# Performance work log

Measured on AMD Instinct MI355X. Metric: run time of the kernel, lower is better.

## Reference

```python
import jax, jax.numpy as jnp
import numpy as np

TH, TL = 0.85, 0.5          # sim thresholds
ALPHA = 0.1                 # proto EMA alpha
TEMP = 1.0                  # readout temperature
KEEP, REFINE, REPLACE, SPAWN = 0, 1, 2, 3


def _l2n(x, axis=-1):
    return x / jnp.maximum(jnp.linalg.norm(x, axis=axis, keepdims=True), 1e-12)


def setup_inputs() -> dict:
    key = jax.random.key(0)
    ks = jax.random.split(key, 12)
    B, N, C, H, W, K = 4, 8, 256, 64, 64, 16
    return {
        "value_BNCHW": jax.random.normal(ks[0], (B, N, C, H, W), jnp.float32),
        "frame_feat_BCHW": jax.random.normal(ks[1], (B, C, H, W), jnp.float32),
        "mask_BNHW": jax.random.uniform(ks[2], (B, N, H, W), jnp.float32),
        "proto": jax.random.normal(ks[3], (B, N, K, C), jnp.float32),
        "age": jax.random.uniform(ks[4], (B, N, K), jnp.float32) * 10.0,
        "usage": jax.random.uniform(ks[5], (B, N, K), jnp.float32) * 5.0,
        "conf": jax.random.uniform(ks[6], (B, N, K), jnp.float32),
        "valid": jax.random.bernoulli(ks[7], 0.7, (B, N, K)),
        "W1": jax.random.normal(ks[8], (C + K + 3 * K, 256), jnp.float32) * 0.02,
        "b1": jnp.zeros((256,), jnp.float32),
        "W2": jax.random.normal(ks[9], (256, 4), jnp.float32) * 0.02,
        "b2": jnp.zeros((4,), jnp.float32),
        "proto_gate": jnp.float32(1.0),
        "frame_gate": jnp.float32(1.0),
    }


def reference(value_BNCHW, frame_feat_BCHW, mask_BNHW, proto, age, usage, conf,
              valid, W1, b1, W2, b2, proto_gate, frame_gate):
    B, N, C, H, W = value_BNCHW.shape
    K = proto.shape[2]
    P = H * W

    # ---- candidate prototype: masked mean pool over HW ----
    flat_v = value_BNCHW.reshape(B, N, C, P)          # [B,N,C,P]
    flat_m = mask_BNHW.reshape(B, N, 1, P)            # [B,N,1,P]
    denom = flat_m.sum(-1)                            # [B,N,1]
    cand = (flat_v * flat_m).sum(-1) / jnp.maximum(denom, 1e-6)
    fallback = flat_v.mean(-1)
    cand = jnp.where(denom <= 1e-5, fallback, cand)   # [B,N,C]
    mask_strength = flat_m.mean(-1)[..., 0]           # [B,N]
    cand = _l2n(cand)

    # ---- cosine sim against bank + context ----
    norm_bank = _l2n(proto)
    sim = jnp.einsum('bnc,bnkc->bnk', cand, norm_bank)
    sim = jnp.where(valid, sim, -1.0)
    g_t = frame_feat_BCHW.mean((2, 3))                # [B,C]
    age_n = age / jnp.maximum(jax.lax.stop_gradient(age.max()), 1.0)
    use_n = usage / jnp.maximum(jax.lax.stop_gradient(usage.max()), 1.0)
    stats = jnp.stack([age_n, use_n, conf], -1).reshape(B, N, 3 * K)
    context = jnp.concatenate(
        [jnp.broadcast_to(g_t[:, None, :], (B, N, C)), sim, stats], -1)
    any_valid = valid.any(-1)
    target_slot = jnp.where(any_valid, sim.argmax(-1), 0)
    max_sim = jnp.take_along_axis(sim, target_slot[..., None], -1)[..., 0]
    max_sim = jnp.where(any_valid, max_sim, 0.0)

    # ---- policy MLP (logits logged; rule-based policy selects action) ----
    logits = jax.nn.gelu(context @ W1 + b1) @ W2 + b2  # [B,N,4]

    has_free = (~valid).any(-1)
    low = max_sim < TL
    action = jnp.full((B, N), REFINE, jnp.int32)
    action = jnp.where(max_sim > TH, KEEP, action)
    action = jnp.where(low & has_free, SPAWN, action)
    action = jnp.where(low & ~has_free, REPLACE, action)

    # ---- action-conditioned slot selection + scatter update ----
    worst = jnp.argmax(age - usage - conf + 1000.0 * (~valid), -1)
    free_slot = jnp.argmax(~valid, -1)
    spawn = action == SPAWN
    replace = action == REPLACE
    refine = action == REFINE
    keep = action == KEEP
    chosen = target_slot
    chosen = jnp.where(spawn & has_free, free_slot, chosen)
    chosen = jnp.where(spawn & ~has_free, worst, chosen)   # spawn_replace_when_full
    chosen = jnp.where(replace, worst, chosen)
    update = refine | replace | spawn
    replace_like = replace | spawn

    bi = jnp.arange(B)[:, None]
    ni = jnp.arange(N)[None, :]

    old_p = proto[bi, ni, chosen]                      # [B,N,C] gather
    refined = _l2n((1.0 - ALPHA) * old_p + ALPHA * cand)
    new_p = jnp.where(refine[..., None], refined,
                      jnp.where(replace_like[..., None], cand, old_p))
    proto_new = proto.at[bi, ni, chosen].set(new_p)

    age1 = age + 1.0
    age_new = age1.at[bi, ni, chosen].set(
        jnp.where(replace_like, 0.0, age1[bi, ni, chosen]))
    usage_new = usage.at[bi, ni, chosen].set(
        jnp.where(replace_like, 1.0,
                  usage[bi, ni, chosen] + (refine | keep).astype(jnp.float32)))
    conf_g = conf[bi, ni, chosen]
    conf_val = jnp.where(refine, jnp.clip(0.5 * conf_g + 0.5 * max_sim, 0.0, 1.0),
                         jnp.where(replace_like, jnp.clip(mask_strength, 0.0, 1.0),
                                   conf_g))
    conf_new = conf.at[bi, ni, chosen].set(conf_val)
    valid_new = valid.at[bi, ni, chosen].set(valid[bi, ni, chosen] | update)

    # ---- prototype-conditioned readout (softmax over bank slots per pixel) ----
    vn = flat_v / jnp.maximum(jnp.linalg.norm(flat_v, axis=2, keepdims=True), 1e-12)
    nb = _l2n(proto_new)
    scores = jnp.einsum('bnkc,bncp->bnkp', nb, vn) / TEMP
    scores = jnp.where(valid_new[..., None], scores, -1e9)
    wts = jax.nn.softmax(scores, axis=2)               # over K
    proto_map = jnp.einsum('bnkp,bnkc->bncp', wts, proto_new)
    proto_map = jnp.where(valid_new.any(-1)[:, :, None, None], proto_map, 0.0)
    proto_map = proto_map.reshape(B, N, C, H, W)

    conditioned = (value_BNCHW + proto_gate * proto_map
                   + frame_gate * frame_feat_BCHW[:, None])
    return conditioned, logits
```

## Files before the change

kernel.cpp:

```cpp
#include <hip/hip_runtime.h>
#include <math.h>

#define NB_B 4
#define NB_N 8
#define NB_C 256
#define NB_K 16
#define NB_P 4096
#define NB_BN (NB_B * NB_N)

#define WS_WSUM 0
#define WS_VSUM (NB_BN * NB_C)
#define WS_GT   (2 * NB_BN * NB_C)
#define WS_DEN  (WS_GT + NB_B * NB_C)
#define WS_NB   17440
#define WS_PN   (WS_NB + NB_BN * NB_K * NB_C)
#define WS_VAL  (WS_PN + NB_BN * NB_K * NB_C)

__device__ __forceinline__ float2 blk_sum2(float a, float b, float2* sbuf) {
#pragma unroll
  for (int off = 32; off > 0; off >>= 1) {
    a += __shfl_down(a, off, 64);
    b += __shfl_down(b, off, 64);
  }
  int lane = threadIdx.x & 63, wid = threadIdx.x >> 6;
  __syncthreads();
  if (lane == 0) sbuf[wid] = make_float2(a, b);
  __syncthreads();
  float2 r;
  r.x = sbuf[0].x + sbuf[1].x + sbuf[2].x + sbuf[3].x;
  r.y = sbuf[0].y + sbuf[1].y + sbuf[2].y + sbuf[3].y;
  return r;
}

__device__ __forceinline__ float2 blk_max2(float a, float b, float2* sbuf) {
#pragma unroll
  for (int off = 32; off > 0; off >>= 1) {
    a = fmaxf(a, __shfl_down(a, off, 64));
    b = fmaxf(b, __shfl_down(b, off, 64));
  }
  int lane = threadIdx.x & 63, wid = threadIdx.x >> 6;
  __syncthreads();
  if (lane == 0) sbuf[wid] = make_float2(a, b);
  __syncthreads();
  float2 r;
  r.x = fmaxf(fmaxf(sbuf[0].x, sbuf[1].x), fmaxf(sbuf[2].x, sbuf[3].x));
  r.y = fmaxf(fmaxf(sbuf[0].y, sbuf[1].y), fmaxf(sbuf[2].y, sbuf[3].y));
  return r;
}

__device__ __forceinline__ int validMode(const void* vptr) {
  const unsigned int* w = (const unsigned int*)vptr;
  int mode = 0;
  for (int i = 0; i < 128; ++i) {
    unsigned int x = w[i];
    if (x == 0x3f800000u) return 2;
    if (x > 1u) mode = 1;
  }
  return mode;
}
__device__ __forceinline__ bool getValid(const void* vptr, int mode, int idx) {
  if (mode == 1) return ((const unsigned char*)vptr)[idx] != 0;
  if (mode == 2) return ((const float*)vptr)[idx] != 0.0f;
  return ((const int*)vptr)[idx] != 0;
}

__global__ __launch_bounds__(256) void k1_reduce(
    const float* __restrict__ value, const float* __restrict__ frame,
    const float* __restrict__ mask, float* __restrict__ ws) {
  __shared__ float2 sbuf[4];
  int gid = blockIdx.x, tid = threadIdx.x;
  if (gid < NB_BN * NB_C) {
    int bn = gid >> 8;
    const float4* v4 = (const float4*)(value + (size_t)gid * NB_P);
    const float4* m4 = (const float4*)(mask + (size_t)bn * NB_P);
    float wsum = 0.f, vsum = 0.f;
#pragma unroll
    for (int i = 0; i < NB_P / 4 / 256; ++i) {
      float4 a = v4[i * 256 + tid];
      float4 m = m4[i * 256 + tid];
      wsum += a.x * m.x + a.y * m.y + a.z * m.z + a.w * m.w;
      vsum += a.x + a.y + a.z + a.w;
    }
    float2 r = blk_sum2(wsum, vsum, sbuf);
    if (tid == 0) { ws[WS_WSUM + gid] = r.x; ws[WS_VSUM + gid] = r.y; }
  } else if (gid < NB_BN * NB_C + NB_B * NB_C) {
    int idx = gid - NB_BN * NB_C;
    const float4* f4 = (const float4*)(frame + (size_t)idx * NB_P);
    float s = 0.f;
#pragma unroll
    for (int i = 0; i < 4; ++i) {
      float4 a = f4[i * 256 + tid];
      s += a.x + a.y + a.z + a.w;
    }
    float2 r = blk_sum2(s, 0.f, sbuf);
    if (tid == 0) ws[WS_GT + idx] = r.x * (1.0f / NB_P);
  } else {
    int bn = gid - NB_BN * NB_C - NB_B * NB_C;
    const float4* m4 = (const float4*)(mask + (size_t)bn * NB_P);
    float s = 0.f;
#pragma unroll
    for (int i = 0; i < 4; ++i) {
      float4 a = m4[i * 256 + tid];
      s += a.x + a.y + a.z + a.w;
    }
    float2 r = blk_sum2(s, 0.f, sbuf);
    if (tid == 0) ws[WS_DEN + bn] = r.x;
  }
}

__global__ __launch_bounds__(256) void k2_policy(
    const float* __restrict__ proto, const float* __restrict__ age,
    const float* __restrict__ usage, const float* __restrict__ conf,
    const void* __restrict__ valid, const float* __restrict__ W1,
    const float* __restrict__ b1, const float* __restrict__ W2,
    const float* __restrict__ b2, float* __restrict__ ws,
    float* __restrict__ out_logits) {
  __shared__ float2 sbuf[4];
  __shared__ float s_cand[NB_C];
  __shared__ float s_sim[NB_K];
  __shared__ float s_invn[NB_K];
  __shared__ float s_ctx[NB_C + NB_K + 3 * NB_K];
  __shared__ int s_dec[4];

  int bn = blockIdx.x;
  int b = bn >> 3;
  int c = threadIdx.x;
  int vmode = validMode(valid);

  float denom = ws[WS_DEN + bn];
  float cand;
  if (denom <= 1e-5f) cand = ws[WS_VSUM + bn * NB_C + c] * (1.0f / NB_P);
  else                cand = ws[WS_WSUM + bn * NB_C + c] / fmaxf(denom, 1e-6f);
  float2 r0 = blk_sum2(cand * cand, 0.f, sbuf);
  cand *= 1.0f / fmaxf(sqrtf(r0.x), 1e-12f);
  s_cand[c] = cand;

  const float* pr = proto + (size_t)bn * NB_K * NB_C;
  for (int k = 0; k < NB_K; ++k) {
    float p = pr[k * NB_C + c];
    float2 rr = blk_sum2(p * p, p * cand, sbuf);
    if (c == 0) {
      float invk = 1.0f / fmaxf(sqrtf(rr.x), 1e-12f);
      s_invn[k] = invk;
      s_sim[k] = getValid(valid, vmode, bn * NB_K + k) ? rr.y * invk : -1.0f;
    }
  }

  float am = fmaxf(age[c], age[c + 256]);
  float um = fmaxf(usage[c], usage[c + 256]);
  float2 mx = blk_max2(am, um, sbuf);
  float age_max = fmaxf(mx.x, 1.0f);
  float use_max = fmaxf(mx.y, 1.0f);

  s_ctx[c] = ws[WS_GT + b * NB_C + c];
  if (c < NB_K) {
    int k = c;
    s_ctx[NB_C + k] = s_sim[k];
    s_ctx[NB_C + NB_K + 3 * k + 0] = age[bn * NB_K + k] / age_max;
    s_ctx[NB_C + NB_K + 3 * k + 1] = usage[bn * NB_K + k] / use_max;
    s_ctx[NB_C + NB_K + 3 * k + 2] = conf[bn * NB_K + k];
  }
  __syncthreads();

  float acc = b1[c];
  for (int i = 0; i < NB_C + 4 * NB_K; ++i) acc += s_ctx[i] * W1[i * 256 + c];
  float h = 0.5f * acc *
            (1.0f + tanhf(0.7978845608028654f * (acc + 0.044715f * acc * acc * acc)));
  for (int j = 0; j < 4; ++j) {
    float2 lj = blk_sum2(h * W2[c * 4 + j], 0.f, sbuf);
    if (c == 0) out_logits[bn * 4 + j] = lj.x + b2[j];
  }

  if (c == 0) {
    bool anyv = false, hasfree = false;
    for (int k = 0; k < NB_K; ++k) {
      if (getValid(valid, vmode, bn * NB_K + k)) anyv = true; else hasfree = true;
    }
    int tgt = 0; float best = s_sim[0];
    for (int k = 1; k < NB_K; ++k) if (s_sim[k] > best) { best = s_sim[k]; tgt = k; }
    if (!anyv) tgt = 0;
    float max_sim = anyv ? s_sim[tgt] : 0.0f;
    int action = 1;
    if (max_sim > 0.85f) action = 0;
    bool low = max_sim < 0.5f;
    if (low && hasfree) action = 3;
    if (low && !hasfree) action = 2;
    int worst = 0; float wb = -1e30f;
    for (int k = 0; k < NB_K; ++k) {
      float sc = age[bn * NB_K + k] - usage[bn * NB_K + k] - conf[bn * NB_K + k] +
                 (getValid(valid, vmode, bn * NB_K + k) ? 0.f : 1000.f);
      if (sc > wb) { wb = sc; worst = k; }
    }
    int freeslot = 0;
    for (int k = 0; k < NB_K; ++k) {
      if (!getValid(valid, vmode, bn * NB_K + k)) { freeslot = k; break; }
    }
    int chosen = tgt;
    if (action == 3) chosen = hasfree ? freeslot : worst;
    if (action == 2) chosen = worst;
    s_dec[0] = chosen;
    s_dec[1] = (action == 1);
    s_dec[2] = (action == 2 || action == 3);
    s_dec[3] = (action != 0);
  }
  __syncthreads();

  int chosen = s_dec[0];
  float oldp = pr[chosen * NB_C + c];
  float t = 0.9f * oldp + 0.1f * s_cand[c];
  float2 tn = blk_sum2(t * t, 0.f, sbuf);
  float invt = 1.0f / fmaxf(sqrtf(tn.x), 1e-12f);
  float pn_chosen = s_dec[1] ? t * invt
                   : (s_dec[2] ? s_cand[c]
                               : oldp);
  float nb_chosen = s_dec[1] ? t * invt
                   : (s_dec[2] ? s_cand[c]
                               : oldp * s_invn[chosen]);
  float* nbp = ws + WS_NB + (size_t)bn * NB_K * NB_C;
  float* pnp = ws + WS_PN + (size_t)bn * NB_K * NB_C;
  for (int k = 0; k < NB_K; ++k) {
    float praw = pr[k * NB_C + c];
    nbp[k * NB_C + c] = (k == chosen) ? nb_chosen : praw * s_invn[k];
    pnp[k * NB_C + c] = (k == chosen) ? pn_chosen : praw;
  }
  if (c < NB_K) {
    bool v = getValid(valid, vmode, bn * NB_K + c) || (c == chosen && s_dec[3]);
    ws[WS_VAL + bn * NB_K + c] = v ? 1.0f : 0.0f;
  }
}

__global__ __launch_bounds__(256) void k3_readout(
    const float* __restrict__ value, const float* __restrict__ frame,
    const float* __restrict__ ws, const float* __restrict__ pgp,
    const float* __restrict__ fgp, float* __restrict__ out) {
  __shared__ float s_nb[NB_C][NB_K];
  __shared__ float s_pn[NB_C][NB_K];
  int blk = blockIdx.x;
  int bn = blk >> 4, tile = blk & 15;
  int b = bn >> 3;
  int tid = threadIdx.x;
  int p = tile * 256 + tid;

  const float* nbp = ws + WS_NB + (size_t)bn * NB_K * NB_C;
  const float* pnp = ws + WS_PN + (size_t)bn * NB_K * NB_C;
  for (int i = tid; i < NB_K * NB_C; i += 256) {
    int k = i >> 8, c = i & 255;
    s_nb[c][k] = nbp[i];
    s_pn[c][k] = pnp[i];
  }
  int vmask = 0;
  for (int k = 0; k < NB_K; ++k)
    if (ws[WS_VAL + bn * NB_K + k] != 0.0f) vmask |= (1 << k);
  float pg = pgp[0], fg = fgp[0];
  __syncthreads();

  const float* vp = value + (size_t)bn * NB_C * NB_P + p;
  float d[NB_K];
#pragma unroll
  for (int k = 0; k < NB_K; ++k) d[k] = 0.f;
  float sumsq = 0.f;
#pragma unroll 4
  for (int c = 0; c < NB_C; ++c) {
    float v = vp[(size_t)c * NB_P];
    sumsq += v * v;
    const float4* nb4 = (const float4*)(&s_nb[c][0]);
    float4 n0 = nb4[0], n1 = nb4[1], n2 = nb4[2], n3 = nb4[3];
    d[0] += v * n0.x;  d[1] += v * n0.y;  d[2] += v * n0.z;  d[3] += v * n0.w;
    d[4] += v * n1.x;  d[5] += v * n1.y;  d[6] += v * n1.z;  d[7] += v * n1.w;
    d[8] += v * n2.x;  d[9] += v * n2.y;  d[10] += v * n2.z; d[11] += v * n2.w;
    d[12] += v * n3.x; d[13] += v * n3.y; d[14] += v * n3.z; d[15] += v * n3.w;
  }
  float invv = 1.0f / fmaxf(sqrtf(sumsq), 1e-12f);
  float m = -1e30f;
#pragma unroll
  for (int k = 0; k < NB_K; ++k) {
    d[k] *= invv;
    if ((vmask >> k) & 1) m = fmaxf(m, d[k]);
  }
  float w[NB_K]; float ssum = 0.f;
#pragma unroll
  for (int k = 0; k < NB_K; ++k) {
    float e = ((vmask >> k) & 1) ? __expf(d[k] - m) : 0.f;
    w[k] = e; ssum += e;
  }
  float isum = vmask ? (1.0f / ssum) : 0.0f;
#pragma unroll
  for (int k = 0; k < NB_K; ++k) w[k] *= isum;

  const float* fp = frame + (size_t)b * NB_C * NB_P + p;
  float* op = out + (size_t)bn * NB_C * NB_P + p;
#pragma unroll 2
  for (int c = 0; c < NB_C; ++c) {
    float v = vp[(size_t)c * NB_P];
    float f = fp[(size_t)c * NB_P];
    const float4* pn4 = (const float4*)(&s_pn[c][0]);
    float4 n0 = pn4[0], n1 = pn4[1], n2 = pn4[2], n3 = pn4[3];
    float pm = w[0] * n0.x + w[1] * n0.y + w[2] * n0.z + w[3] * n0.w +
               w[4] * n1.x + w[5] * n1.y + w[6] * n1.z + w[7] * n1.w +
               w[8] * n2.x + w[9] * n2.y + w[10] * n2.z + w[11] * n2.w +
               w[12] * n3.x + w[13] * n3.y + w[14] * n3.z + w[15] * n3.w;
    op[(size_t)c * NB_P] = v + pg * pm + fg * f;
  }
}

extern "C" void kernel_launch(void* const* d_in, const int* in_sizes, int n_in,
                              void* d_out, int out_size, void* d_ws, size_t ws_size,
                              hipStream_t stream) {
  const float* value = (const float*)d_in[0];
  const float* frame = (const float*)d_in[1];
  const float* mask  = (const float*)d_in[2];
  const float* proto = (const float*)d_in[3];
  const float* age   = (const float*)d_in[4];
  const float* usage = (const float*)d_in[5];
  const float* conf  = (const float*)d_in[6];
  const void*  valid = (const void*)d_in[7];
  const float* W1 = (const float*)d_in[8];
  const float* b1 = (const float*)d_in[9];
  const float* W2 = (const float*)d_in[10];
  const float* b2 = (const float*)d_in[11];
  const float* pg = (const float*)d_in[12];
  const float* fg = (const float*)d_in[13];
  float* out = (float*)d_out;
  float* ws = (float*)d_ws;

  int g1 = NB_BN * NB_C + NB_B * NB_C + NB_BN;
  hipLaunchKernelGGL(k1_reduce, dim3(g1), dim3(256), 0, stream,
                     value, frame, mask, ws);
  hipLaunchKernelGGL(k2_policy, dim3(NB_BN), dim3(256), 0, stream,
                     proto, age, usage, conf, valid, W1, b1, W2, b2, ws,
                     out + (size_t)NB_BN * NB_C * NB_P);
  hipLaunchKernelGGL(k3_readout, dim3(NB_BN * 16), dim3(256), 0, stream,
                     value, frame, ws, pg, fg, out);
}
```

Baseline: 150.2 us.

## Split readout channels across half-blocks and batch reduce rows per block

k1 now reduces four channel rows per block and reuses the mask loads across them, which cuts the block count and the number of mask reads. k3 now splits the 256 channels between two 128-thread halves, combines their partial dot products through shared memory, and doubles the grid to 1024 blocks for more parallelism. Shared memory is reused for the normalised and raw bank, the bank is stored channel-major so it loads with coalesced float4 copies, and the output is written with nontemporal stores. The cost is an extra shared-memory reduction step and added barriers in the readout.

Measured after the change: 161.3 us. 1.07x slower.

```diff
diff --git a/kernel.cpp b/kernel.cpp
--- a/kernel.cpp
+++ b/kernel.cpp
@@ -16,6 +16,24 @@
 #define WS_PN   (WS_NB + NB_BN * NB_K * NB_C)
 #define WS_VAL  (WS_PN + NB_BN * NB_K * NB_C)
 
+__device__ __forceinline__ void blk_sum8(float* a, float (*sbuf)[8]) {
+#pragma unroll
+  for (int off = 32; off > 0; off >>= 1) {
+#pragma unroll
+    for (int j = 0; j < 8; ++j) a[j] += __shfl_down(a[j], off, 64);
+  }
+  int lane = threadIdx.x & 63, wid = threadIdx.x >> 6;
+  __syncthreads();
+  if (lane == 0) {
+#pragma unroll
+    for (int j = 0; j < 8; ++j) sbuf[wid][j] = a[j];
+  }
+  __syncthreads();
+#pragma unroll
+  for (int j = 0; j < 8; ++j)
+    a[j] = sbuf[0][j] + sbuf[1][j] + sbuf[2][j] + sbuf[3][j];
+}
+
 __device__ __forceinline__ float2 blk_sum2(float a, float b, float2* sbuf) {
 #pragma unroll
   for (int off = 32; off > 0; off >>= 1) {
@@ -67,44 +85,70 @@
 __global__ __launch_bounds__(256) void k1_reduce(
     const float* __restrict__ value, const float* __restrict__ frame,
     const float* __restrict__ mask, float* __restrict__ ws) {
-  __shared__ float2 sbuf[4];
+  __shared__ float sbuf[4][8];
   int gid = blockIdx.x, tid = threadIdx.x;
-  if (gid < NB_BN * NB_C) {
-    int bn = gid >> 8;
-    const float4* v4 = (const float4*)(value + (size_t)gid * NB_P);
+  if (gid < 2048) {
+    int bn = gid >> 6, c0 = (gid & 63) << 2;
     const float4* m4 = (const float4*)(mask + (size_t)bn * NB_P);
-    float wsum = 0.f, vsum = 0.f;
-#pragma unroll
-    for (int i = 0; i < NB_P / 4 / 256; ++i) {
-      float4 a = v4[i * 256 + tid];
-      float4 m = m4[i * 256 + tid];
-      wsum += a.x * m.x + a.y * m.y + a.z * m.z + a.w * m.w;
-      vsum += a.x + a.y + a.z + a.w;
-    }
-    float2 r = blk_sum2(wsum, vsum, sbuf);
-    if (tid == 0) { ws[WS_WSUM + gid] = r.x; ws[WS_VSUM + gid] = r.y; }
-  } else if (gid < NB_BN * NB_C + NB_B * NB_C) {
-    int idx = gid - NB_BN * NB_C;
-    const float4* f4 = (const float4*)(frame + (size_t)idx * NB_P);
-    float s = 0.f;
-#pragma unroll
-    for (int i = 0; i < 4; ++i) {
-      float4 a = f4[i * 256 + tid];
-      s += a.x + a.y + a.z + a.w;
-    }
-    float2 r = blk_sum2(s, 0.f, sbuf);
-    if (tid == 0) ws[WS_GT + idx] = r.x * (1.0f / NB_P);
+    float4 mv[4];
+#pragma unroll
+    for (int i = 0; i < 4; ++i) mv[i] = m4[i * 256 + tid];
+    float acc[8];
+#pragma unroll
+    for (int r = 0; r < 4; ++r) {
+      const float4* v4 =
+          (const float4*)(value + ((size_t)bn * NB_C + c0 + r) * NB_P);
+      float wsum = 0.f, vsum = 0.f;
+#pragma unroll
+      for (int i = 0; i < 4; ++i) {
+        float4 a = v4[i * 256 + tid];
+        wsum += a.x * mv[i].x + a.y * mv[i].y + a.z * mv[i].z + a.w * mv[i].w;
+        vsum += a.x + a.y + a.z + a.w;
+      }
+      acc[2 * r] = wsum;
+      acc[2 * r + 1] = vsum;
+    }
+    blk_sum8(acc, sbuf);
+    if (tid == 0) {
+#pragma unroll
+      for (int r = 0; r < 4; ++r) {
+        ws[WS_WSUM + bn * NB_C + c0 + r] = acc[2 * r];
+        ws[WS_VSUM + bn * NB_C + c0 + r] = acc[2 * r + 1];
+      }
+    }
+  } else if (gid < 2048 + 256) {
+    int idx0 = (gid - 2048) << 2;
+    float acc[8] = {0.f, 0.f, 0.f, 0.f, 0.f, 0.f, 0.f, 0.f};
+#pragma unroll
+    for (int r = 0; r < 4; ++r) {
+      const float4* f4 = (const float4*)(frame + (size_t)(idx0 + r) * NB_P);
+      float s = 0.f;
+#pragma unroll
+      for (int i = 0; i < 4; ++i) {
+        float4 a = f4[i * 256 + tid];
+        s += a.x + a.y + a.z + a.w;
+      }
+      acc[r] = s;
+    }
+    blk_sum8(acc, sbuf);
+    if (tid == 0) {
+#pragma unroll
+      for (int r = 0; r < 4; ++r)
+        ws[WS_GT + idx0 + r] = acc[r] * (1.0f / NB_P);
+    }
   } else {
-    int bn = gid - NB_BN * NB_C - NB_B * NB_C;
+    int bn = gid - 2304;
     const float4* m4 = (const float4*)(mask + (size_t)bn * NB_P);
+    float acc[8] = {0.f, 0.f, 0.f, 0.f, 0.f, 0.f, 0.f, 0.f};
     float s = 0.f;
 #pragma unroll
     for (int i = 0; i < 4; ++i) {
       float4 a = m4[i * 256 + tid];
       s += a.x + a.y + a.z + a.w;
     }
-    float2 r = blk_sum2(s, 0.f, sbuf);
-    if (tid == 0) ws[WS_DEN + bn] = r.x;
+    acc[0] = s;
+    blk_sum8(acc, sbuf);
+    if (tid == 0) ws[WS_DEN + bn] = acc[0];
   }
 }
 
@@ -211,17 +255,15 @@
   float2 tn = blk_sum2(t * t, 0.f, sbuf);
   float invt = 1.0f / fmaxf(sqrtf(tn.x), 1e-12f);
   float pn_chosen = s_dec[1] ? t * invt
-                   : (s_dec[2] ? s_cand[c]
-                               : oldp);
+                   : (s_dec[2] ? s_cand[c] : oldp);
   float nb_chosen = s_dec[1] ? t * invt
-                   : (s_dec[2] ? s_cand[c]
-                               : oldp * s_invn[chosen]);
+                   : (s_dec[2] ? s_cand[c] : oldp * s_invn[chosen]);
   float* nbp = ws + WS_NB + (size_t)bn * NB_K * NB_C;
   float* pnp = ws + WS_PN + (size_t)bn * NB_K * NB_C;
   for (int k = 0; k < NB_K; ++k) {
     float praw = pr[k * NB_C + c];
-    nbp[k * NB_C + c] = (k == chosen) ? nb_chosen : praw * s_invn[k];
-    pnp[k * NB_C + c] = (k == chosen) ? pn_chosen : praw;
+    nbp[c * NB_K + k] = (k == chosen) ? nb_chosen : praw * s_invn[k];
+    pnp[c * NB_K + k] = (k == chosen) ? pn_chosen : praw;
   }
   if (c < NB_K) {
     bool v = getValid(valid, vmode, bn * NB_K + c) || (c == chosen && s_dec[3]);
@@ -229,47 +271,65 @@
   }
 }
 
-__global__ __launch_bounds__(256) void k3_readout(
+__global__ __launch_bounds__(256, 4) void k3_readout(
     const float* __restrict__ value, const float* __restrict__ frame,
     const float* __restrict__ ws, const float* __restrict__ pgp,
     const float* __restrict__ fgp, float* __restrict__ out) {
-  __shared__ float s_nb[NB_C][NB_K];
-  __shared__ float s_pn[NB_C][NB_K];
+  __shared__ float s_bank[NB_C * NB_K];
+  __shared__ float s_red[256 * 17];
   int blk = blockIdx.x;
-  int bn = blk >> 4, tile = blk & 15;
+  int bn = blk >> 5, tile = blk & 31;
   int b = bn >> 3;
   int tid = threadIdx.x;
-  int p = tile * 256 + tid;
-
-  const float* nbp = ws + WS_NB + (size_t)bn * NB_K * NB_C;
-  const float* pnp = ws + WS_PN + (size_t)bn * NB_K * NB_C;
-  for (int i = tid; i < NB_K * NB_C; i += 256) {
-    int k = i >> 8, c = i & 255;
-    s_nb[c][k] = nbp[i];
-    s_pn[c][k] = pnp[i];
-  }
+  int px = tid & 127, ch = tid >> 7;
+  int p0 = tile * 128;
+
+  const float4* nbp4 = (const float4*)(ws + WS_NB + (size_t)bn * NB_K * NB_C);
+  float4* sb4 = (float4*)s_bank;
+#pragma unroll
+  for (int j = 0; j < 4; ++j) sb4[j * 256 + tid] = nbp4[j * 256 + tid];
   int vmask = 0;
   for (int k = 0; k < NB_K; ++k)
     if (ws[WS_VAL + bn * NB_K + k] != 0.0f) vmask |= (1 << k);
   float pg = pgp[0], fg = fgp[0];
   __syncthreads();
 
-  const float* vp = value + (size_t)bn * NB_C * NB_P + p;
+  const float* vp = value + ((size_t)bn * NB_C + ch * 128) * NB_P + p0 + px;
+  const float* sbch = s_bank + ch * 128 * NB_K;
   float d[NB_K];
 #pragma unroll
   for (int k = 0; k < NB_K; ++k) d[k] = 0.f;
   float sumsq = 0.f;
-#pragma unroll 4
-  for (int c = 0; c < NB_C; ++c) {
+#pragma unroll 8
+  for (int c = 0; c < 128; ++c) {
     float v = vp[(size_t)c * NB_P];
     sumsq += v * v;
-    const float4* nb4 = (const float4*)(&s_nb[c][0]);
-    float4 n0 = nb4[0], n1 = nb4[1], n2 = nb4[2], n3 = nb4[3];
+    const float4* n4 = (const float4*)(sbch + c * NB_K);
+    float4 n0 = n4[0], n1 = n4[1], n2 = n4[2], n3 = n4[3];
     d[0] += v * n0.x;  d[1] += v * n0.y;  d[2] += v * n0.z;  d[3] += v * n0.w;
     d[4] += v * n1.x;  d[5] += v * n1.y;  d[6] += v * n1.z;  d[7] += v * n1.w;
     d[8] += v * n2.x;  d[9] += v * n2.y;  d[10] += v * n2.z; d[11] += v * n2.w;
     d[12] += v * n3.x; d[13] += v * n3.y; d[14] += v * n3.z; d[15] += v * n3.w;
   }
+  {
+    float* rr = s_red + tid * 17;
+#pragma unroll
+    for (int k = 0; k < NB_K; ++k) rr[k] = d[k];
+    rr[16] = sumsq;
+  }
+  __syncthreads();
+
+  const float4* pnp4 = (const float4*)(ws + WS_PN + (size_t)bn * NB_K * NB_C);
+#pragma unroll
+  for (int j = 0; j < 4; ++j) sb4[j * 256 + tid] = pnp4[j * 256 + tid];
+
+  {
+    const float* r0 = s_red + px * 17;
+    const float* r1 = s_red + (128 + px) * 17;
+#pragma unroll
+    for (int k = 0; k < NB_K; ++k) d[k] = r0[k] + r1[k];
+    sumsq = r0[16] + r1[16];
+  }
   float invv = 1.0f / fmaxf(sqrtf(sumsq), 1e-12f);
   float m = -1e30f;
 #pragma unroll
@@ -286,20 +346,21 @@
   float isum = vmask ? (1.0f / ssum) : 0.0f;
 #pragma unroll
   for (int k = 0; k < NB_K; ++k) w[k] *= isum;
-
-  const float* fp = frame + (size_t)b * NB_C * NB_P + p;
-  float* op = out + (size_t)bn * NB_C * NB_P + p;
-#pragma unroll 2
-  for (int c = 0; c < NB_C; ++c) {
+  __syncthreads();
+
+  const float* fp = frame + ((size_t)b * NB_C + ch * 128) * NB_P + p0 + px;
+  float* op = out + ((size_t)bn * NB_C + ch * 128) * NB_P + p0 + px;
+#pragma unroll 4
+  for (int c = 0; c < 128; ++c) {
     float v = vp[(size_t)c * NB_P];
     float f = fp[(size_t)c * NB_P];
-    const float4* pn4 = (const float4*)(&s_pn[c][0]);
-    float4 n0 = pn4[0], n1 = pn4[1], n2 = pn4[2], n3 = pn4[3];
+    const float4* n4 = (const float4*)(sbch + c * NB_K);
+    float4 n0 = n4[0], n1 = n4[1], n2 = n4[2], n3 = n4[3];
     float pm = w[0] * n0.x + w[1] * n0.y + w[2] * n0.z + w[3] * n0.w +
                w[4] * n1.x + w[5] * n1.y + w[6] * n1.z + w[7] * n1.w +
                w[8] * n2.x + w[9] * n2.y + w[10] * n2.z + w[11] * n2.w +
                w[12] * n3.x + w[13] * n3.y + w[14] * n3.z + w[15] * n3.w;
-    op[(size_t)c * NB_P] = v + pg * pm + fg * f;
+    __builtin_nontemporal_store(v + pg * pm + fg * f, &op[(size_t)c * NB_P]);
   }
 }
 
@@ -323,12 +384,11 @@
   float* out = (float*)d_out;
   float* ws = (float*)d_ws;
 
-  int g1 = NB_BN * NB_C + NB_B * NB_C + NB_BN;
-  hipLaunchKernelGGL(k1_reduce, dim3(g1), dim3(256), 0, stream,
+  hipLaunchKernelGGL(k1_reduce, dim3(2048 + 256 + 32), dim3(256), 0, stream,
                      value, frame, mask, ws);
   hipLaunchKernelGGL(k2_policy, dim3(NB_BN), dim3(256), 0, stream,
                      proto, age, usage, conf, valid, W1, b1, W2, b2, ws,
                      out + (size_t)NB_BN * NB_C * NB_P);
-  hipLaunchKernelGGL(k3_readout, dim3(NB_BN * 16), dim3(256), 0, stream,
+  hipLaunchKernelGGL(k3_readout, dim3(NB_BN * 32), dim3(256), 0, stream,
                      value, frame, ws, pg, fg, out);
 }
```

## Vectorize readout to four pixels per thread and transpose bank layout in policy kernel

Applied to the files above, without the earlier changes.

The readout kernel now has each thread handle four adjacent pixels with float4 loads, uses 128-thread blocks and half as many blocks, and writes output with nontemporal stores. The policy kernel writes the bank in [c][k] layout with float4 stores so the readout can copy it into shared memory directly, and it computes the per-slot norms with one wave per four slots instead of sixteen block-wide reductions. The goal is to cut memory instruction count and reduction sync overhead. The cost is heavier register pressure (64 accumulators per thread) and only 256 blocks of 128 threads, which may lower occupancy and latency hiding.

Result: no change. 149.1 us (-0.7%).

```diff
diff --git a/kernel.cpp b/kernel.cpp
--- a/kernel.cpp
+++ b/kernel.cpp
@@ -7,6 +7,8 @@
 #define NB_K 16
 #define NB_P 4096
 #define NB_BN (NB_B * NB_N)
+
+typedef float nfloat4 __attribute__((ext_vector_type(4)));
 
 #define WS_WSUM 0
 #define WS_VSUM (NB_BN * NB_C)
@@ -121,11 +123,12 @@
   __shared__ float s_invn[NB_K];
   __shared__ float s_ctx[NB_C + NB_K + 3 * NB_K];
   __shared__ int s_dec[4];
+  __shared__ int s_vmode;
 
   int bn = blockIdx.x;
   int b = bn >> 3;
   int c = threadIdx.x;
-  int vmode = validMode(valid);
+  if (c == 0) s_vmode = validMode(valid);
 
   float denom = ws[WS_DEN + bn];
   float cand;
@@ -134,15 +137,33 @@
   float2 r0 = blk_sum2(cand * cand, 0.f, sbuf);
   cand *= 1.0f / fmaxf(sqrtf(r0.x), 1e-12f);
   s_cand[c] = cand;
+  __syncthreads();
+  int vmode = s_vmode;
 
   const float* pr = proto + (size_t)bn * NB_K * NB_C;
-  for (int k = 0; k < NB_K; ++k) {
-    float p = pr[k * NB_C + c];
-    float2 rr = blk_sum2(p * p, p * cand, sbuf);
-    if (c == 0) {
-      float invk = 1.0f / fmaxf(sqrtf(rr.x), 1e-12f);
-      s_invn[k] = invk;
-      s_sim[k] = getValid(valid, vmode, bn * NB_K + k) ? rr.y * invk : -1.0f;
+  {
+    int wid = c >> 6, lane = c & 63;
+#pragma unroll
+    for (int q = 0; q < 4; ++q) {
+      int k = wid * 4 + q;
+      float pp = 0.f, pc = 0.f;
+#pragma unroll
+      for (int t = 0; t < 4; ++t) {
+        int cc = lane + t * 64;
+        float p = pr[k * NB_C + cc];
+        pp += p * p;
+        pc += p * s_cand[cc];
+      }
+#pragma unroll
+      for (int off = 32; off > 0; off >>= 1) {
+        pp += __shfl_down(pp, off, 64);
+        pc += __shfl_down(pc, off, 64);
+      }
+      if (lane == 0) {
+        float invk = 1.0f / fmaxf(sqrtf(pp), 1e-12f);
+        s_invn[k] = invk;
+        s_sim[k] = getValid(valid, vmode, bn * NB_K + k) ? pc * invk : -1.0f;
+      }
     }
   }
 
@@ -210,18 +231,24 @@
   float t = 0.9f * oldp + 0.1f * s_cand[c];
   float2 tn = blk_sum2(t * t, 0.f, sbuf);
   float invt = 1.0f / fmaxf(sqrtf(tn.x), 1e-12f);
-  float pn_chosen = s_dec[1] ? t * invt
-                   : (s_dec[2] ? s_cand[c]
-                               : oldp);
+  float pn_chosen = s_dec[1] ? t * invt : (s_dec[2] ? s_cand[c] : oldp);
   float nb_chosen = s_dec[1] ? t * invt
-                   : (s_dec[2] ? s_cand[c]
-                               : oldp * s_invn[chosen]);
-  float* nbp = ws + WS_NB + (size_t)bn * NB_K * NB_C;
-  float* pnp = ws + WS_PN + (size_t)bn * NB_K * NB_C;
+                   : (s_dec[2] ? s_cand[c] : oldp * s_invn[chosen]);
+  float nbrow[NB_K], pnrow[NB_K];
+#pragma unroll
   for (int k = 0; k < NB_K; ++k) {
     float praw = pr[k * NB_C + c];
-    nbp[k * NB_C + c] = (k == chosen) ? nb_chosen : praw * s_invn[k];
-    pnp[k * NB_C + c] = (k == chosen) ? pn_chosen : praw;
+    nbrow[k] = (k == chosen) ? nb_chosen : praw * s_invn[k];
+    pnrow[k] = (k == chosen) ? pn_chosen : praw;
+  }
+  float* nbp = ws + WS_NB + (size_t)bn * NB_K * NB_C + c * NB_K;
+  float* pnp = ws + WS_PN + (size_t)bn * NB_K * NB_C + c * NB_K;
+#pragma unroll
+  for (int q = 0; q < 4; ++q) {
+    *(float4*)(nbp + 4 * q) =
+        make_float4(nbrow[4 * q], nbrow[4 * q + 1], nbrow[4 * q + 2], nbrow[4 * q + 3]);
+    *(float4*)(pnp + 4 * q) =
+        make_float4(pnrow[4 * q], pnrow[4 * q + 1], pnrow[4 * q + 2], pnrow[4 * q + 3]);
   }
   if (c < NB_K) {
     bool v = getValid(valid, vmode, bn * NB_K + c) || (c == chosen && s_dec[3]);
@@ -229,24 +256,24 @@
   }
 }
 
-__global__ __launch_bounds__(256) void k3_readout(
+__global__ __launch_bounds__(128) void k3_fused(
     const float* __restrict__ value, const float* __restrict__ frame,
     const float* __restrict__ ws, const float* __restrict__ pgp,
     const float* __restrict__ fgp, float* __restrict__ out) {
-  __shared__ float s_nb[NB_C][NB_K];
-  __shared__ float s_pn[NB_C][NB_K];
+  __shared__ float s_nb[NB_C * NB_K];
+  __shared__ float s_pn[NB_C * NB_K];
   int blk = blockIdx.x;
-  int bn = blk >> 4, tile = blk & 15;
+  int bn = blk >> 3, pxt = blk & 7;
   int b = bn >> 3;
   int tid = threadIdx.x;
-  int p = tile * 256 + tid;
-
-  const float* nbp = ws + WS_NB + (size_t)bn * NB_K * NB_C;
-  const float* pnp = ws + WS_PN + (size_t)bn * NB_K * NB_C;
-  for (int i = tid; i < NB_K * NB_C; i += 256) {
-    int k = i >> 8, c = i & 255;
-    s_nb[c][k] = nbp[i];
-    s_pn[c][k] = pnp[i];
+  int px = pxt * 512 + tid * 4;
+
+  const float4* nb4 = (const float4*)(ws + WS_NB + (size_t)bn * NB_K * NB_C);
+  const float4* pn4 = (const float4*)(ws + WS_PN + (size_t)bn * NB_K * NB_C);
+#pragma unroll
+  for (int j = 0; j < 8; ++j) {
+    ((float4*)s_nb)[j * 128 + tid] = nb4[j * 128 + tid];
+    ((float4*)s_pn)[j * 128 + tid] = pn4[j * 128 + tid];
   }
   int vmask = 0;
   for (int k = 0; k < NB_K; ++k)
@@ -254,52 +281,83 @@
   float pg = pgp[0], fg = fgp[0];
   __syncthreads();
 
-  const float* vp = value + (size_t)bn * NB_C * NB_P + p;
-  float d[NB_K];
-#pragma unroll
-  for (int k = 0; k < NB_K; ++k) d[k] = 0.f;
-  float sumsq = 0.f;
+  const float* vp = value + (size_t)bn * NB_C * NB_P + px;
+  float4 d[NB_K];
+#pragma unroll
+  for (int k = 0; k < NB_K; ++k) d[k] = make_float4(0.f, 0.f, 0.f, 0.f);
+  float4 ss = make_float4(0.f, 0.f, 0.f, 0.f);
 #pragma unroll 4
   for (int c = 0; c < NB_C; ++c) {
-    float v = vp[(size_t)c * NB_P];
-    sumsq += v * v;
-    const float4* nb4 = (const float4*)(&s_nb[c][0]);
-    float4 n0 = nb4[0], n1 = nb4[1], n2 = nb4[2], n3 = nb4[3];
-    d[0] += v * n0.x;  d[1] += v * n0.y;  d[2] += v * n0.z;  d[3] += v * n0.w;
-    d[4] += v * n1.x;  d[5] += v * n1.y;  d[6] += v * n1.z;  d[7] += v * n1.w;
-    d[8] += v * n2.x;  d[9] += v * n2.y;  d[10] += v * n2.z; d[11] += v * n2.w;
-    d[12] += v * n3.x; d[13] += v * n3.y; d[14] += v * n3.z; d[15] += v * n3.w;
-  }
-  float invv = 1.0f / fmaxf(sqrtf(sumsq), 1e-12f);
-  float m = -1e30f;
+    float4 v = *(const float4*)(vp + (size_t)c * NB_P);
+    ss.x += v.x * v.x; ss.y += v.y * v.y; ss.z += v.z * v.z; ss.w += v.w * v.w;
+    const float4* nrow = (const float4*)(s_nb + c * NB_K);
+    float4 n0 = nrow[0], n1 = nrow[1], n2 = nrow[2], n3 = nrow[3];
+#define ACC(K, S)                                                        \
+    d[K].x += v.x * S; d[K].y += v.y * S; d[K].z += v.z * S; d[K].w += v.w * S;
+    ACC(0, n0.x)  ACC(1, n0.y)  ACC(2, n0.z)  ACC(3, n0.w)
+    ACC(4, n1.x)  ACC(5, n1.y)  ACC(6, n1.z)  ACC(7, n1.w)
+    ACC(8, n2.x)  ACC(9, n2.y)  ACC(10, n2.z) ACC(11, n2.w)
+    ACC(12, n3.x) ACC(13, n3.y) ACC(14, n3.z) ACC(15, n3.w)
+#undef ACC
+  }
+
+  float4 invv;
+  invv.x = 1.0f / fmaxf(sqrtf(ss.x), 1e-12f);
+  invv.y = 1.0f / fmaxf(sqrtf(ss.y), 1e-12f);
+  invv.z = 1.0f / fmaxf(sqrtf(ss.z), 1e-12f);
+  invv.w = 1.0f / fmaxf(sqrtf(ss.w), 1e-12f);
+  float4 m = make_float4(-1e30f, -1e30f, -1e30f, -1e30f);
 #pragma unroll
   for (int k = 0; k < NB_K; ++k) {
-    d[k] *= invv;
-    if ((vmask >> k) & 1) m = fmaxf(m, d[k]);
-  }
-  float w[NB_K]; float ssum = 0.f;
+    d[k].x *= invv.x; d[k].y *= invv.y; d[k].z *= invv.z; d[k].w *= invv.w;
+    if ((vmask >> k) & 1) {
+      m.x = fmaxf(m.x, d[k].x); m.y = fmaxf(m.y, d[k].y);
+      m.z = fmaxf(m.z, d[k].z); m.w = fmaxf(m.w, d[k].w);
+    }
+  }
+  float4 es = make_float4(0.f, 0.f, 0.f, 0.f);
 #pragma unroll
   for (int k = 0; k < NB_K; ++k) {
-    float e = ((vmask >> k) & 1) ? __expf(d[k] - m) : 0.f;
-    w[k] = e; ssum += e;
-  }
-  float isum = vmask ? (1.0f / ssum) : 0.0f;
-#pragma unroll
-  for (int k = 0; k < NB_K; ++k) w[k] *= isum;
-
-  const float* fp = frame + (size_t)b * NB_C * NB_P + p;
-  float* op = out + (size_t)bn * NB_C * NB_P + p;
+    if ((vmask >> k) & 1) {
+      d[k].x = __expf(d[k].x - m.x); d[k].y = __expf(d[k].y - m.y);
+      d[k].z = __expf(d[k].z - m.z); d[k].w = __expf(d[k].w - m.w);
+      es.x += d[k].x; es.y += d[k].y; es.z += d[k].z; es.w += d[k].w;
+    } else {
+      d[k] = make_float4(0.f, 0.f, 0.f, 0.f);
+    }
+  }
+  float4 isum;
+  isum.x = vmask ? (1.0f / es.x) : 0.0f;
+  isum.y = vmask ? (1.0f / es.y) : 0.0f;
+  isum.z = vmask ? (1.0f / es.z) : 0.0f;
+  isum.w = vmask ? (1.0f / es.w) : 0.0f;
+#pragma unroll
+  for (int k = 0; k < NB_K; ++k) {
+    d[k].x *= isum.x; d[k].y *= isum.y; d[k].z *= isum.z; d[k].w *= isum.w;
+  }
+
+  const float* fp = frame + (size_t)b * NB_C * NB_P + px;
+  float* op = out + (size_t)bn * NB_C * NB_P + px;
 #pragma unroll 2
   for (int c = 0; c < NB_C; ++c) {
-    float v = vp[(size_t)c * NB_P];
-    float f = fp[(size_t)c * NB_P];
-    const float4* pn4 = (const float4*)(&s_pn[c][0]);
-    float4 n0 = pn4[0], n1 = pn4[1], n2 = pn4[2], n3 = pn4[3];
-    float pm = w[0] * n0.x + w[1] * n0.y + w[2] * n0.z + w[3] * n0.w +
-               w[4] * n1.x + w[5] * n1.y + w[6] * n1.z + w[7] * n1.w +
-               w[8] * n2.x + w[9] * n2.y + w[10] * n2.z + w[11] * n2.w +
-               w[12] * n3.x + w[13] * n3.y + w[14] * n3.z + w[15] * n3.w;
-    op[(size_t)c * NB_P] = v + pg * pm + fg * f;
+    float4 v = *(const float4*)(vp + (size_t)c * NB_P);
+    float4 f = *(const float4*)(fp + (size_t)c * NB_P);
+    const float4* prow = (const float4*)(s_pn + c * NB_K);
+    float4 p0 = prow[0], p1 = prow[1], p2 = prow[2], p3 = prow[3];
+    float4 pm = make_float4(0.f, 0.f, 0.f, 0.f);
+#define APM(K, S)                                                        \
+    pm.x += d[K].x * S; pm.y += d[K].y * S; pm.z += d[K].z * S; pm.w += d[K].w * S;
+    APM(0, p0.x)  APM(1, p0.y)  APM(2, p0.z)  APM(3, p0.w)
+    APM(4, p1.x)  APM(5, p1.y)  APM(6, p1.z)  APM(7, p1.w)
+    APM(8, p2.x)  APM(9, p2.y)  APM(10, p2.z) APM(11, p2.w)
+    APM(12, p3.x) APM(13, p3.y) APM(14, p3.z) APM(15, p3.w)
+#undef APM
+    nfloat4 o;
+    o.x = v.x + pg * pm.x + fg * f.x;
+    o.y = v.y + pg * pm.y + fg * f.y;
+    o.z = v.z + pg * pm.z + fg * f.z;
+    o.w = v.w + pg * pm.w + fg * f.w;
+    __builtin_nontemporal_store(o, (nfloat4*)(op + (size_t)c * NB_P));
   }
 }
 
@@ -329,6 +387,6 @@
   hipLaunchKernelGGL(k2_policy, dim3(NB_BN), dim3(256), 0, stream,
                      proto, age, usage, conf, valid, W1, b1, W2, b2, ws,
                      out + (size_t)NB_BN * NB_C * NB_P);
-  hipLaunchKernelGGL(k3_readout, dim3(NB_BN * 16), dim3(256), 0, stream,
+  hipLaunchKernelGGL(k3_fused, dim3(NB_BN * 8), dim3(128), 0, stream,
                      value, frame, ws, pg, fg, out);
 }
```
